# Kernel optimization log

Measured on AMD Instinct MI355X. Metric: run time of the kernel, lower is better.

Reference implementation:

```python
import jax, jax.numpy as jnp
import numpy as np

NUM_HEADS = 32
HEAD_DIM = 128
LORA_RANK = 512
Q_LORA_RANK = 1536
BSZ = 16
SEQ_LEN = 4096


def setup_inputs() -> dict:
    key = jax.random.key(0)
    k1, k2, k3, k4, k5, k6 = jax.random.split(key, 6)
    hd = NUM_HEADS * HEAD_DIM
    return {
        "hidden_states_q": jax.random.normal(k1, (BSZ, Q_LORA_RANK), dtype=jnp.float32),
        "compressed_kv": jax.random.normal(k2, (BSZ, SEQ_LEN, LORA_RANK), dtype=jnp.float32),
        # nn.Linear params: weight [out, in], bias [out]
        "Wq": jax.random.normal(k3, (hd, Q_LORA_RANK), dtype=jnp.float32) / np.sqrt(Q_LORA_RANK),
        "bq": jax.random.normal(k4, (hd,), dtype=jnp.float32) * 0.01,
        "Wkv": jax.random.normal(k5, (hd, LORA_RANK), dtype=jnp.float32) / np.sqrt(LORA_RANK),
        "bkv": jax.random.normal(k6, (hd,), dtype=jnp.float32) * 0.01,
    }


def reference(hidden_states_q, compressed_kv, Wq, bq, Wkv, bkv):
    bsz = hidden_states_q.shape[0]
    seq_len = compressed_kv.shape[1]
    # q: [b, h, d]
    q = (hidden_states_q @ Wq.T + bq).reshape(bsz, NUM_HEADS, HEAD_DIM)
    # kv decompression: [b, s, h, d] (same tensor used for both K and V)
    kv = (compressed_kv @ Wkv.T + bkv).reshape(bsz, seq_len, NUM_HEADS, HEAD_DIM)
    # attention scores per head over seq (note: original has NO 1/sqrt(d) scaling)
    attn = jnp.einsum('bhd,bshd->bhs', q, kv)
    attn = jax.nn.softmax(attn, axis=-1)
    out = jnp.einsum('bhs,bshd->bhd', attn, kv)
    return out.reshape(bsz, NUM_HEADS * HEAD_DIM)
```

## Files before the change

### kernel.cpp

```cpp
#include <hip/hip_runtime.h>

#define B  16
#define S  4096
#define R  512
#define QR 1536
#define H  32
#define D  128
#define HD 4096
#define SC 128
#define CH 32

using f32x4 = __attribute__((ext_vector_type(4))) float;
using s16x8 = __attribute__((ext_vector_type(8))) short;

__device__ __forceinline__ ushort bf_hi(float x) {
  return (ushort)(__float_as_uint(x) >> 16);
}
__device__ __forceinline__ float bf_res(float x) {
  return x - __uint_as_float(__float_as_uint(x) & 0xFFFF0000u);
}
__device__ __forceinline__ ushort f2bf_rne(float x) {
  uint u = __float_as_uint(x);
  return (ushort)((u + 0x7FFFu + ((u >> 16) & 1u)) >> 16);
}

__global__ __launch_bounds__(512) void k_q(const float* __restrict__ hsq,
                                           const float* __restrict__ Wq,
                                           const float* __restrict__ bq,
                                           float* __restrict__ q) {
  __shared__ float hs[B * QR];
  int tid = threadIdx.x;
  for (int idx = tid * 4; idx < B * QR; idx += 2048)
    *(float4*)&hs[idx] = *(const float4*)&hsq[idx];
  __syncthreads();

  int wave = tid >> 6, lane = tid & 63;
  int o = blockIdx.x * 16 + wave * 2;

  float acc0[B], acc1[B];
#pragma unroll
  for (int b = 0; b < B; ++b) { acc0[b] = 0.f; acc1[b] = 0.f; }

  const float* w0r = Wq + (size_t)o * QR;
  const float* w1r = w0r + QR;
  for (int k = lane * 4; k < QR; k += 256) {
    float4 wa = *(const float4*)&w0r[k];
    float4 wb = *(const float4*)&w1r[k];
#pragma unroll
    for (int b = 0; b < B; ++b) {
      float4 h4 = *(const float4*)&hs[b * QR + k];
      acc0[b] += wa.x * h4.x + wa.y * h4.y + wa.z * h4.z + wa.w * h4.w;
      acc1[b] += wb.x * h4.x + wb.y * h4.y + wb.z * h4.z + wb.w * h4.w;
    }
  }
#pragma unroll
  for (int b = 0; b < B; ++b) {
    float v0 = acc0[b], v1 = acc1[b];
#pragma unroll
    for (int off = 32; off > 0; off >>= 1) {
      v0 += __shfl_xor(v0, off);
      v1 += __shfl_xor(v1, off);
    }
    if (lane == 0) {
      q[b * HD + o]     = v0 + bq[o];
      q[b * HD + o + 1] = v1 + bq[o + 1];
    }
  }
}

__global__ __launch_bounds__(256) void k_qhat(const float* __restrict__ q,
                                              const float* __restrict__ Wkv,
                                              float* __restrict__ qhat) {
  int h = blockIdx.x;
  int r0 = blockIdx.y * 64;
  __shared__ float qs[B][D];
  int tid = threadIdx.x;
  for (int idx = tid; idx < B * D; idx += 256) {
    int b = idx >> 7, d = idx & (D - 1);
    qs[b][d] = q[b * HD + h * D + d];
  }
  __syncthreads();

  int r_l = tid & 63, bg = tid >> 6;
  float acc[4] = {0.f, 0.f, 0.f, 0.f};
  const float* wbase = Wkv + (size_t)(h * D) * R + r0 + r_l;
  for (int d = 0; d < D; d += 4) {
    float w0 = wbase[(d + 0) * R];
    float w1 = wbase[(d + 1) * R];
    float w2 = wbase[(d + 2) * R];
    float w3 = wbase[(d + 3) * R];
#pragma unroll
    for (int i = 0; i < 4; ++i) {
      float4 q4 = *(const float4*)&qs[bg * 4 + i][d];
      acc[i] += q4.x * w0 + q4.y * w1 + q4.z * w2 + q4.w * w3;
    }
  }
#pragma unroll
  for (int i = 0; i < 4; ++i)
    qhat[((size_t)(bg * 4 + i) * H + h) * R + r0 + r_l] = acc[i];
}

__global__ __launch_bounds__(256) void k_fmha(const float* __restrict__ qhat,
                                              const float* __restrict__ ckv,
                                              float* __restrict__ part,
                                              float* __restrict__ mbuf,
                                              float* __restrict__ lbuf) {
  __shared__ __align__(16) ushort cs1h[SC * 64];
  __shared__ __align__(16) ushort cs1l[SC * 64];
  __shared__ __align__(16) float  Ls[H * 132];
  __shared__ __align__(16) ushort Ps[H * 128];
  __shared__ __align__(16) ushort cs2[64 * SC];

  const int b = blockIdx.x, chunk = blockIdx.y;
  const int tid = threadIdx.x;
  const int lane = tid & 63, w = tid >> 6;
  const float* cbase = ckv + ((size_t)b * S + (size_t)chunk * SC) * R;
  const float* qbase = qhat + (size_t)b * H * R;

  f32x4 acc[2][2];
#pragma unroll
  for (int i = 0; i < 2; ++i)
#pragma unroll
    for (int j = 0; j < 2; ++j) acc[i][j] = {0.f, 0.f, 0.f, 0.f};

  const int st_s = tid >> 1;
  const int st_kh = (tid & 1) * 32;

  for (int kt = 0; kt < R; kt += 64) {
    {
      const float* src = cbase + (size_t)st_s * R + kt + st_kh;
#pragma unroll
      for (int j = 0; j < 8; ++j) {
        float4 v = *(const float4*)(src + 4 * j);
        int k0 = st_kh + 4 * j;
        int idx = st_s * 64 + (((k0 >> 3) ^ (st_s & 7)) << 3) + (k0 & 7);
        *(uint*)&cs1h[idx]     = (uint)bf_hi(v.x) | ((uint)bf_hi(v.y) << 16);
        *(uint*)&cs1h[idx + 2] = (uint)bf_hi(v.z) | ((uint)bf_hi(v.w) << 16);
        *(uint*)&cs1l[idx]     = (uint)bf_hi(bf_res(v.x)) | ((uint)bf_hi(bf_res(v.y)) << 16);
        *(uint*)&cs1l[idx + 2] = (uint)bf_hi(bf_res(v.z)) | ((uint)bf_hi(bf_res(v.w)) << 16);
      }
    }
    __syncthreads();
#pragma unroll
    for (int ks = 0; ks < 2; ++ks) {
      const int kk = kt + ks * 32 + (lane >> 4) * 8;
      s16x8 ah[2], al[2], bh[2], bl[2];
#pragma unroll
      for (int mt = 0; mt < 2; ++mt) {
        const float* qp = qbase + (size_t)((lane & 15) + 16 * mt) * R + kk;
        float4 q0 = *(const float4*)qp;
        float4 q1 = *(const float4*)(qp + 4);
        float qv[8] = {q0.x, q0.y, q0.z, q0.w, q1.x, q1.y, q1.z, q1.w};
        s16x8 th, tl;
#pragma unroll
        for (int e = 0; e < 8; ++e) {
          th[e] = (short)bf_hi(qv[e]);
          tl[e] = (short)bf_hi(bf_res(qv[e]));
        }
        ah[mt] = th; al[mt] = tl;
      }
#pragma unroll
      for (int ntl = 0; ntl < 2; ++ntl) {
        int sf = (lane & 15) + 32 * w + 16 * ntl;
        int kb = ks * 4 + (lane >> 4);
        int idx = sf * 64 + ((kb ^ (sf & 7)) << 3);
        bh[ntl] = *(s16x8*)&cs1h[idx];
        bl[ntl] = *(s16x8*)&cs1l[idx];
      }
#pragma unroll
      for (int mt = 0; mt < 2; ++mt)
#pragma unroll
        for (int ntl = 0; ntl < 2; ++ntl) {
          acc[mt][ntl] = __builtin_amdgcn_mfma_f32_16x16x32_bf16(ah[mt], bh[ntl], acc[mt][ntl], 0, 0, 0);
          acc[mt][ntl] = __builtin_amdgcn_mfma_f32_16x16x32_bf16(ah[mt], bl[ntl], acc[mt][ntl], 0, 0, 0);
          acc[mt][ntl] = __builtin_amdgcn_mfma_f32_16x16x32_bf16(al[mt], bh[ntl], acc[mt][ntl], 0, 0, 0);
        }
    }
    __syncthreads();
  }

#pragma unroll
  for (int mt = 0; mt < 2; ++mt)
#pragma unroll
    for (int ntl = 0; ntl < 2; ++ntl)
#pragma unroll
      for (int i = 0; i < 4; ++i) {
        int row = 16 * mt + (lane >> 4) * 4 + i;
        int col = 32 * w + 16 * ntl + (lane & 15);
        Ls[row * 132 + col] = acc[mt][ntl][i];
      }
  __syncthreads();

  {
    const int h = tid >> 3, sl = tid & 7;
    float vals[16];
    float m = -3.0e38f;
#pragma unroll
    for (int k = 0; k < 16; ++k) {
      vals[k] = Ls[h * 132 + sl + 8 * k];
      m = fmaxf(m, vals[k]);
    }
    m = fmaxf(m, __shfl_xor(m, 1));
    m = fmaxf(m, __shfl_xor(m, 2));
    m = fmaxf(m, __shfl_xor(m, 4));
    float sum = 0.f;
#pragma unroll
    for (int k = 0; k < 16; ++k) {
      float e = __expf(vals[k] - m);
      sum += e;
      Ps[h * 128 + ((k ^ (h & 7)) << 3) + sl] = f2bf_rne(e);
    }
    sum += __shfl_xor(sum, 1);
    sum += __shfl_xor(sum, 2);
    sum += __shfl_xor(sum, 4);
    if (sl == 0) {
      mbuf[((size_t)b * CH + chunk) * H + h] = m;
      lbuf[((size_t)b * CH + chunk) * H + h] = sum;
    }
  }
  __syncthreads();

  s16x8 bp[4][2];
#pragma unroll
  for (int kt = 0; kt < 4; ++kt)
#pragma unroll
    for (int nt = 0; nt < 2; ++nt) {
      int h = 16 * nt + (lane & 15);
      int kb = kt * 4 + (lane >> 4);
      bp[kt][nt] = *(s16x8*)&Ps[h * 128 + ((kb ^ (h & 7)) << 3)];
    }

  float* pb = part + (size_t)(b * CH + chunk) * H * R;
  const int b7 = tid & 7, sp = tid >> 3;

  for (int rt = 0; rt < 8; ++rt) {
    const int r0 = rt * 64;
#pragma unroll
    for (int so = 0; so < 2; ++so) {
      int s = 2 * sp + 64 * so;
      const float* row0 = cbase + (size_t)s * R + r0;
      const float* row1 = row0 + R;
#pragma unroll
      for (int i = 0; i < 8; ++i) {
        int r = b7 + 8 * i;
        int idx = r * 128 + (((s >> 3) ^ (r & 7)) << 3) + (s & 7);
        *(uint*)&cs2[idx] = (uint)f2bf_rne(row0[r]) | ((uint)f2bf_rne(row1[r]) << 16);
      }
    }
    __syncthreads();

    f32x4 acc2[2];
    acc2[0] = {0.f, 0.f, 0.f, 0.f};
    acc2[1] = {0.f, 0.f, 0.f, 0.f};
    const int rl = 16 * w + (lane & 15);
#pragma unroll
    for (int kt = 0; kt < 4; ++kt) {
      int kb = kt * 4 + (lane >> 4);
      s16x8 a2 = *(s16x8*)&cs2[rl * 128 + ((kb ^ (rl & 7)) << 3)];
#pragma unroll
      for (int nt = 0; nt < 2; ++nt)
        acc2[nt] = __builtin_amdgcn_mfma_f32_16x16x32_bf16(a2, bp[kt][nt], acc2[nt], 0, 0, 0);
    }
#pragma unroll
    for (int nt = 0; nt < 2; ++nt) {
      int h = 16 * nt + (lane & 15);
#pragma unroll
      for (int i = 0; i < 4; ++i) {
        int rg = r0 + 16 * w + (lane >> 4) * 4 + i;
        pb[(size_t)h * R + rg] = acc2[nt][i];
      }
    }
    __syncthreads();
  }
}

__global__ __launch_bounds__(256) void k_combine(const float* __restrict__ part,
                                                 const float* __restrict__ mbuf,
                                                 const float* __restrict__ lbuf,
                                                 float* __restrict__ ctx) {
  const int bid = blockIdx.x;
  const int b = bid >> 5, h = bid & 31;
  const int tid = threadIdx.x;
  float mv[CH], wv[CH];
  float M = -3.0e38f;
#pragma unroll
  for (int c = 0; c < CH; ++c) {
    mv[c] = mbuf[((size_t)b * CH + c) * H + h];
    M = fmaxf(M, mv[c]);
  }
  float denom = 0.f;
#pragma unroll
  for (int c = 0; c < CH; ++c) {
    wv[c] = __expf(mv[c] - M);
    denom += wv[c] * lbuf[((size_t)b * CH + c) * H + h];
  }
  const float inv = 1.f / denom;
  float s0 = 0.f, s1 = 0.f;
#pragma unroll
  for (int c = 0; c < CH; ++c) {
    const float* pp = part + (((size_t)b * CH + c) * H + h) * R;
    s0 += wv[c] * pp[tid];
    s1 += wv[c] * pp[tid + 256];
  }
  ctx[((size_t)b * H + h) * R + tid] = s0 * inv;
  ctx[((size_t)b * H + h) * R + tid + 256] = s1 * inv;
}

__global__ __launch_bounds__(256) void k_out(const float* __restrict__ ctx,
                                             const float* __restrict__ Wkv,
                                             const float* __restrict__ bkv,
                                             float* __restrict__ out) {
  int h = blockIdx.x;
  int d0 = blockIdx.y * 32;
  __shared__ float cs[B][R];
  int tid = threadIdx.x;
  for (int idx = tid * 4; idx < B * R; idx += 1024) {
    int b = idx >> 9, r = idx & 511;
    *(float4*)&cs[b][r] = *(const float4*)&ctx[(size_t)(b * H + h) * R + r];
  }
  __syncthreads();

  int dg = tid & 31;
  int bg = tid >> 5;
  int d = d0 + dg;
  int b0 = bg * 2;
  float acc0 = 0.f, acc1 = 0.f;
  const float* wrow = Wkv + ((size_t)(h * D + d)) * R;
  for (int i = 0; i < R; i += 4) {
    float4 w4 = *(const float4*)&wrow[i];
    float4 ca = *(const float4*)&cs[b0][i];
    float4 cb = *(const float4*)&cs[b0 + 1][i];
    acc0 += w4.x * ca.x + w4.y * ca.y + w4.z * ca.z + w4.w * ca.w;
    acc1 += w4.x * cb.x + w4.y * cb.y + w4.z * cb.z + w4.w * cb.w;
  }
  float bv = bkv[h * D + d];
  out[(size_t)b0 * HD + h * D + d]       = acc0 + bv;
  out[(size_t)(b0 + 1) * HD + h * D + d] = acc1 + bv;
}

extern "C" void kernel_launch(void* const* d_in, const int* in_sizes, int n_in,
                              void* d_out, int out_size, void* d_ws, size_t ws_size,
                              hipStream_t stream) {
  (void)in_sizes; (void)n_in; (void)out_size; (void)ws_size;
  const float* hsq = (const float*)d_in[0];
  const float* ckv = (const float*)d_in[1];
  const float* Wq  = (const float*)d_in[2];
  const float* bq  = (const float*)d_in[3];
  const float* Wkv = (const float*)d_in[4];
  const float* bkv = (const float*)d_in[5];
  float* out = (float*)d_out;

  float* ws   = (float*)d_ws;
  float* q    = ws;
  float* qhat = q + 65536;
  float* ctx  = qhat + 262144;
  float* mbuf = ctx + 262144;
  float* lbuf = mbuf + (size_t)B * CH * H;
  float* part = lbuf + (size_t)B * CH * H;

  k_q<<<256, 512, 0, stream>>>(hsq, Wq, bq, q);
  k_qhat<<<dim3(32, 8), 256, 0, stream>>>(q, Wkv, qhat);
  k_fmha<<<dim3(B, CH), 256, 0, stream>>>(qhat, ckv, part, mbuf, lbuf);
  k_combine<<<B * H, 256, 0, stream>>>(part, mbuf, lbuf, ctx);
  k_out<<<dim3(32, 4), 256, 0, stream>>>(ctx, Wkv, bkv, out);
}
```

Before: 106.3 us.

## Restructure fused attention kernel: 512 threads, register prefetch, bf16 partials

The attention kernel grows to 512 threads per block. The next K-tile and V-tile are prefetched into registers while the current tile is computed, and q is staged once per tile through shared memory in split bf16 instead of being reconverted by every wave. Softmax now uses in-register shuffle reductions instead of a shared-memory score matrix, and LDS buffers are aliased to save space. Partial outputs are stored as bf16 to halve the write and read traffic between the attention and combine kernels, which adds rounding error to the partial sums.

```diff
diff --git a/kernel.cpp b/kernel.cpp
--- a/kernel.cpp
+++ b/kernel.cpp
@@ -22,6 +22,9 @@
 __device__ __forceinline__ ushort f2bf_rne(float x) {
   uint u = __float_as_uint(x);
   return (ushort)((u + 0x7FFFu + ((u >> 16) & 1u)) >> 16);
+}
+__device__ __forceinline__ float bf2f(ushort u) {
+  return __uint_as_float((uint)u << 16);
 }
 
 __global__ __launch_bounds__(512) void k_q(const float* __restrict__ hsq,
@@ -100,181 +103,230 @@
     qhat[((size_t)(bg * 4 + i) * H + h) * R + r0 + r_l] = acc[i];
 }
 
-__global__ __launch_bounds__(256) void k_fmha(const float* __restrict__ qhat,
-                                              const float* __restrict__ ckv,
-                                              float* __restrict__ part,
-                                              float* __restrict__ mbuf,
-                                              float* __restrict__ lbuf) {
-  __shared__ __align__(16) ushort cs1h[SC * 64];
-  __shared__ __align__(16) ushort cs1l[SC * 64];
-  __shared__ __align__(16) float  Ls[H * 132];
+__global__ __launch_bounds__(512, 4) void k_fmha(const float* __restrict__ qhat,
+                                                 const float* __restrict__ ckv,
+                                                 ushort* __restrict__ part,
+                                                 float* __restrict__ mbuf,
+                                                 float* __restrict__ lbuf) {
+  __shared__ __align__(16) ushort smem[24576];
   __shared__ __align__(16) ushort Ps[H * 128];
-  __shared__ __align__(16) ushort cs2[64 * SC];
+
+  ushort* cs1h = smem;
+  ushort* cs1l = smem + 8192;
+  ushort* qsh  = smem + 16384;
+  ushort* qsl  = smem + 20480;
+  float*  redm = (float*)(smem + 8192);
+  float*  redl = redm + 256;
+  ushort* cs2  = smem;
 
   const int b = blockIdx.x, chunk = blockIdx.y;
   const int tid = threadIdx.x;
   const int lane = tid & 63, w = tid >> 6;
+  const int lcol = lane & 15, lgrp = lane >> 4;
   const float* cbase = ckv + ((size_t)b * S + (size_t)chunk * SC) * R;
   const float* qbase = qhat + (size_t)b * H * R;
 
-  f32x4 acc[2][2];
-#pragma unroll
-  for (int i = 0; i < 2; ++i)
-#pragma unroll
-    for (int j = 0; j < 2; ++j) acc[i][j] = {0.f, 0.f, 0.f, 0.f};
-
-  const int st_s = tid >> 1;
-  const int st_kh = (tid & 1) * 32;
+  const int st_s = tid >> 2;
+  const int st_k = (tid & 3) * 16;
+  const int qrow = tid >> 4;
+  const int qk   = (tid & 15) * 4;
+
+  f32x4 acc[2];
+  acc[0] = {0.f, 0.f, 0.f, 0.f};
+  acc[1] = {0.f, 0.f, 0.f, 0.f};
+
+  float4 v[4], vq;
+  {
+    const float* src = cbase + (size_t)st_s * R + st_k;
+#pragma unroll
+    for (int j = 0; j < 4; ++j) v[j] = *(const float4*)(src + 4 * j);
+    vq = *(const float4*)(qbase + (size_t)qrow * R + qk);
+  }
 
   for (int kt = 0; kt < R; kt += 64) {
+#pragma unroll
+    for (int j = 0; j < 4; ++j) {
+      int k0 = st_k + 4 * j;
+      int idx = st_s * 64 + (((k0 >> 3) ^ (st_s & 7)) << 3) + (k0 & 7);
+      float4 t = v[j];
+      *(uint*)&cs1h[idx]     = (uint)bf_hi(t.x) | ((uint)bf_hi(t.y) << 16);
+      *(uint*)&cs1h[idx + 2] = (uint)bf_hi(t.z) | ((uint)bf_hi(t.w) << 16);
+      *(uint*)&cs1l[idx]     = (uint)bf_hi(bf_res(t.x)) | ((uint)bf_hi(bf_res(t.y)) << 16);
+      *(uint*)&cs1l[idx + 2] = (uint)bf_hi(bf_res(t.z)) | ((uint)bf_hi(bf_res(t.w)) << 16);
+    }
     {
-      const float* src = cbase + (size_t)st_s * R + kt + st_kh;
-#pragma unroll
-      for (int j = 0; j < 8; ++j) {
-        float4 v = *(const float4*)(src + 4 * j);
-        int k0 = st_kh + 4 * j;
-        int idx = st_s * 64 + (((k0 >> 3) ^ (st_s & 7)) << 3) + (k0 & 7);
-        *(uint*)&cs1h[idx]     = (uint)bf_hi(v.x) | ((uint)bf_hi(v.y) << 16);
-        *(uint*)&cs1h[idx + 2] = (uint)bf_hi(v.z) | ((uint)bf_hi(v.w) << 16);
-        *(uint*)&cs1l[idx]     = (uint)bf_hi(bf_res(v.x)) | ((uint)bf_hi(bf_res(v.y)) << 16);
-        *(uint*)&cs1l[idx + 2] = (uint)bf_hi(bf_res(v.z)) | ((uint)bf_hi(bf_res(v.w)) << 16);
+      int idx = qrow * 64 + (((qk >> 3) ^ (qrow & 7)) << 3) + (qk & 7);
+      *(uint*)&qsh[idx]     = (uint)bf_hi(vq.x) | ((uint)bf_hi(vq.y) << 16);
+      *(uint*)&qsh[idx + 2] = (uint)bf_hi(vq.z) | ((uint)bf_hi(vq.w) << 16);
+      *(uint*)&qsl[idx]     = (uint)bf_hi(bf_res(vq.x)) | ((uint)bf_hi(bf_res(vq.y)) << 16);
+      *(uint*)&qsl[idx + 2] = (uint)bf_hi(bf_res(vq.z)) | ((uint)bf_hi(bf_res(vq.w)) << 16);
+    }
+    __syncthreads();
+    if (kt + 64 < R) {
+      const float* src = cbase + (size_t)st_s * R + (kt + 64) + st_k;
+#pragma unroll
+      for (int j = 0; j < 4; ++j) v[j] = *(const float4*)(src + 4 * j);
+      vq = *(const float4*)(qbase + (size_t)qrow * R + (kt + 64) + qk);
+    }
+#pragma unroll
+    for (int ks = 0; ks < 2; ++ks) {
+      const int kb = ks * 4 + lgrp;
+      s16x8 ah[2], al[2], bh, bl;
+#pragma unroll
+      for (int mt = 0; mt < 2; ++mt) {
+        int m = 16 * mt + lcol;
+        int idx = m * 64 + ((kb ^ (m & 7)) << 3);
+        ah[mt] = *(s16x8*)&qsh[idx];
+        al[mt] = *(s16x8*)&qsl[idx];
       }
+      {
+        int sf = 16 * w + lcol;
+        int idx = sf * 64 + ((kb ^ (sf & 7)) << 3);
+        bh = *(s16x8*)&cs1h[idx];
+        bl = *(s16x8*)&cs1l[idx];
+      }
+#pragma unroll
+      for (int mt = 0; mt < 2; ++mt) {
+        acc[mt] = __builtin_amdgcn_mfma_f32_16x16x32_bf16(ah[mt], bh, acc[mt], 0, 0, 0);
+        acc[mt] = __builtin_amdgcn_mfma_f32_16x16x32_bf16(ah[mt], bl, acc[mt], 0, 0, 0);
+        acc[mt] = __builtin_amdgcn_mfma_f32_16x16x32_bf16(al[mt], bh, acc[mt], 0, 0, 0);
+      }
     }
     __syncthreads();
-#pragma unroll
-    for (int ks = 0; ks < 2; ++ks) {
-      const int kk = kt + ks * 32 + (lane >> 4) * 8;
-      s16x8 ah[2], al[2], bh[2], bl[2];
-#pragma unroll
-      for (int mt = 0; mt < 2; ++mt) {
-        const float* qp = qbase + (size_t)((lane & 15) + 16 * mt) * R + kk;
-        float4 q0 = *(const float4*)qp;
-        float4 q1 = *(const float4*)(qp + 4);
-        float qv[8] = {q0.x, q0.y, q0.z, q0.w, q1.x, q1.y, q1.z, q1.w};
-        s16x8 th, tl;
-#pragma unroll
-        for (int e = 0; e < 8; ++e) {
-          th[e] = (short)bf_hi(qv[e]);
-          tl[e] = (short)bf_hi(bf_res(qv[e]));
-        }
-        ah[mt] = th; al[mt] = tl;
+  }
+
+  float pm[2][4];
+#pragma unroll
+  for (int mt = 0; mt < 2; ++mt)
+#pragma unroll
+    for (int i = 0; i < 4; ++i) pm[mt][i] = acc[mt][i];
+#pragma unroll
+  for (int off = 1; off <= 8; off <<= 1)
+#pragma unroll
+    for (int mt = 0; mt < 2; ++mt)
+#pragma unroll
+      for (int i = 0; i < 4; ++i)
+        pm[mt][i] = fmaxf(pm[mt][i], __shfl_xor(pm[mt][i], off));
+  if (lcol == 0) {
+#pragma unroll
+    for (int mt = 0; mt < 2; ++mt)
+#pragma unroll
+      for (int i = 0; i < 4; ++i)
+        redm[(16 * mt + lgrp * 4 + i) * 8 + w] = pm[mt][i];
+  }
+  __syncthreads();
+
+  float e_[2][4], ps[2][4];
+#pragma unroll
+  for (int mt = 0; mt < 2; ++mt)
+#pragma unroll
+    for (int i = 0; i < 4; ++i) {
+      int h = 16 * mt + lgrp * 4 + i;
+      float4 r0 = *(float4*)&redm[h * 8];
+      float4 r1 = *(float4*)&redm[h * 8 + 4];
+      float m = fmaxf(fmaxf(fmaxf(r0.x, r0.y), fmaxf(r0.z, r0.w)),
+                      fmaxf(fmaxf(r1.x, r1.y), fmaxf(r1.z, r1.w)));
+      float e = __expf(acc[mt][i] - m);
+      e_[mt][i] = e;
+      ps[mt][i] = e;
+    }
+#pragma unroll
+  for (int off = 1; off <= 8; off <<= 1)
+#pragma unroll
+    for (int mt = 0; mt < 2; ++mt)
+#pragma unroll
+      for (int i = 0; i < 4; ++i)
+        ps[mt][i] += __shfl_xor(ps[mt][i], off);
+  if (lcol == 0) {
+#pragma unroll
+    for (int mt = 0; mt < 2; ++mt)
+#pragma unroll
+      for (int i = 0; i < 4; ++i)
+        redl[(16 * mt + lgrp * 4 + i) * 8 + w] = ps[mt][i];
+  }
+#pragma unroll
+  for (int mt = 0; mt < 2; ++mt)
+#pragma unroll
+    for (int i = 0; i < 4; ++i) {
+      int h = 16 * mt + lgrp * 4 + i;
+      int s = 16 * w + lcol;
+      Ps[h * 128 + (((s >> 3) ^ (h & 7)) << 3) + (s & 7)] = f2bf_rne(e_[mt][i]);
+    }
+  __syncthreads();
+
+  if (w == 0 && lcol == 0) {
+#pragma unroll
+    for (int mt = 0; mt < 2; ++mt)
+#pragma unroll
+      for (int i = 0; i < 4; ++i) {
+        int h = 16 * mt + lgrp * 4 + i;
+        float4 r0 = *(float4*)&redm[h * 8];
+        float4 r1 = *(float4*)&redm[h * 8 + 4];
+        float M = fmaxf(fmaxf(fmaxf(r0.x, r0.y), fmaxf(r0.z, r0.w)),
+                        fmaxf(fmaxf(r1.x, r1.y), fmaxf(r1.z, r1.w)));
+        float4 l0 = *(float4*)&redl[h * 8];
+        float4 l1 = *(float4*)&redl[h * 8 + 4];
+        float L = (l0.x + l0.y + l0.z + l0.w) + (l1.x + l1.y + l1.z + l1.w);
+        mbuf[((size_t)b * CH + chunk) * H + h] = M;
+        lbuf[((size_t)b * CH + chunk) * H + h] = L;
       }
-#pragma unroll
-      for (int ntl = 0; ntl < 2; ++ntl) {
-        int sf = (lane & 15) + 32 * w + 16 * ntl;
-        int kb = ks * 4 + (lane >> 4);
-        int idx = sf * 64 + ((kb ^ (sf & 7)) << 3);
-        bh[ntl] = *(s16x8*)&cs1h[idx];
-        bl[ntl] = *(s16x8*)&cs1l[idx];
+  }
+
+  const int nt = w & 1, mtr = w >> 1;
+  s16x8 bp4[4];
+#pragma unroll
+  for (int kt4 = 0; kt4 < 4; ++kt4) {
+    int h = 16 * nt + lcol;
+    int kb = kt4 * 4 + lgrp;
+    bp4[kt4] = *(s16x8*)&Ps[h * 128 + ((kb ^ (h & 7)) << 3)];
+  }
+
+  const int b7 = tid & 7, sp = tid >> 3;
+  const int s0 = 2 * sp;
+  float ra[8], rb[8];
+  {
+    const float* row0 = cbase + (size_t)s0 * R;
+    const float* row1 = row0 + R;
+#pragma unroll
+    for (int i = 0; i < 8; ++i) { ra[i] = row0[b7 + 8 * i]; rb[i] = row1[b7 + 8 * i]; }
+  }
+  ushort* pb = part + (size_t)(b * CH + chunk) * H * R;
+
+  for (int rt = 0; rt < 8; ++rt) {
+#pragma unroll
+    for (int i = 0; i < 8; ++i) {
+      int r = b7 + 8 * i;
+      int idx = r * 128 + (((s0 >> 3) ^ (r & 7)) << 3) + (s0 & 7);
+      *(uint*)&cs2[idx] = (uint)f2bf_rne(ra[i]) | ((uint)f2bf_rne(rb[i]) << 16);
+    }
+    __syncthreads();
+    if (rt < 7) {
+      const float* row0 = cbase + (size_t)s0 * R + (rt + 1) * 64;
+      const float* row1 = row0 + R;
+#pragma unroll
+      for (int i = 0; i < 8; ++i) { ra[i] = row0[b7 + 8 * i]; rb[i] = row1[b7 + 8 * i]; }
+    }
+    f32x4 acc2 = {0.f, 0.f, 0.f, 0.f};
+    const int rl = 16 * mtr + lcol;
+#pragma unroll
+    for (int kt4 = 0; kt4 < 4; ++kt4) {
+      int kb = kt4 * 4 + lgrp;
+      s16x8 a2 = *(s16x8*)&cs2[rl * 128 + ((kb ^ (rl & 7)) << 3)];
+      acc2 = __builtin_amdgcn_mfma_f32_16x16x32_bf16(a2, bp4[kt4], acc2, 0, 0, 0);
+    }
+    {
+      int h = 16 * nt + lcol;
+#pragma unroll
+      for (int i = 0; i < 4; ++i) {
+        int rg = rt * 64 + 16 * mtr + lgrp * 4 + i;
+        pb[(size_t)h * R + rg] = f2bf_rne(acc2[i]);
       }
-#pragma unroll
-      for (int mt = 0; mt < 2; ++mt)
-#pragma unroll
-        for (int ntl = 0; ntl < 2; ++ntl) {
-          acc[mt][ntl] = __builtin_amdgcn_mfma_f32_16x16x32_bf16(ah[mt], bh[ntl], acc[mt][ntl], 0, 0, 0);
-          acc[mt][ntl] = __builtin_amdgcn_mfma_f32_16x16x32_bf16(ah[mt], bl[ntl], acc[mt][ntl], 0, 0, 0);
-          acc[mt][ntl] = __builtin_amdgcn_mfma_f32_16x16x32_bf16(al[mt], bh[ntl], acc[mt][ntl], 0, 0, 0);
-        }
     }
     __syncthreads();
   }
-
-#pragma unroll
-  for (int mt = 0; mt < 2; ++mt)
-#pragma unroll
-    for (int ntl = 0; ntl < 2; ++ntl)
-#pragma unroll
-      for (int i = 0; i < 4; ++i) {
-        int row = 16 * mt + (lane >> 4) * 4 + i;
-        int col = 32 * w + 16 * ntl + (lane & 15);
-        Ls[row * 132 + col] = acc[mt][ntl][i];
-      }
-  __syncthreads();
-
-  {
-    const int h = tid >> 3, sl = tid & 7;
-    float vals[16];
-    float m = -3.0e38f;
-#pragma unroll
-    for (int k = 0; k < 16; ++k) {
-      vals[k] = Ls[h * 132 + sl + 8 * k];
-      m = fmaxf(m, vals[k]);
-    }
-    m = fmaxf(m, __shfl_xor(m, 1));
-    m = fmaxf(m, __shfl_xor(m, 2));
-    m = fmaxf(m, __shfl_xor(m, 4));
-    float sum = 0.f;
-#pragma unroll
-    for (int k = 0; k < 16; ++k) {
-      float e = __expf(vals[k] - m);
-      sum += e;
-      Ps[h * 128 + ((k ^ (h & 7)) << 3) + sl] = f2bf_rne(e);
-    }
-    sum += __shfl_xor(sum, 1);
-    sum += __shfl_xor(sum, 2);
-    sum += __shfl_xor(sum, 4);
-    if (sl == 0) {
-      mbuf[((size_t)b * CH + chunk) * H + h] = m;
-      lbuf[((size_t)b * CH + chunk) * H + h] = sum;
-    }
-  }
-  __syncthreads();
-
-  s16x8 bp[4][2];
-#pragma unroll
-  for (int kt = 0; kt < 4; ++kt)
-#pragma unroll
-    for (int nt = 0; nt < 2; ++nt) {
-      int h = 16 * nt + (lane & 15);
-      int kb = kt * 4 + (lane >> 4);
-      bp[kt][nt] = *(s16x8*)&Ps[h * 128 + ((kb ^ (h & 7)) << 3)];
-    }
-
-  float* pb = part + (size_t)(b * CH + chunk) * H * R;
-  const int b7 = tid & 7, sp = tid >> 3;
-
-  for (int rt = 0; rt < 8; ++rt) {
-    const int r0 = rt * 64;
-#pragma unroll
-    for (int so = 0; so < 2; ++so) {
-      int s = 2 * sp + 64 * so;
-      const float* row0 = cbase + (size_t)s * R + r0;
-      const float* row1 = row0 + R;
-#pragma unroll
-      for (int i = 0; i < 8; ++i) {
-        int r = b7 + 8 * i;
-        int idx = r * 128 + (((s >> 3) ^ (r & 7)) << 3) + (s & 7);
-        *(uint*)&cs2[idx] = (uint)f2bf_rne(row0[r]) | ((uint)f2bf_rne(row1[r]) << 16);
-      }
-    }
-    __syncthreads();
-
-    f32x4 acc2[2];
-    acc2[0] = {0.f, 0.f, 0.f, 0.f};
-    acc2[1] = {0.f, 0.f, 0.f, 0.f};
-    const int rl = 16 * w + (lane & 15);
-#pragma unroll
-    for (int kt = 0; kt < 4; ++kt) {
-      int kb = kt * 4 + (lane >> 4);
-      s16x8 a2 = *(s16x8*)&cs2[rl * 128 + ((kb ^ (rl & 7)) << 3)];
-#pragma unroll
-      for (int nt = 0; nt < 2; ++nt)
-        acc2[nt] = __builtin_amdgcn_mfma_f32_16x16x32_bf16(a2, bp[kt][nt], acc2[nt], 0, 0, 0);
-    }
-#pragma unroll
-    for (int nt = 0; nt < 2; ++nt) {
-      int h = 16 * nt + (lane & 15);
-#pragma unroll
-      for (int i = 0; i < 4; ++i) {
-        int rg = r0 + 16 * w + (lane >> 4) * 4 + i;
-        pb[(size_t)h * R + rg] = acc2[nt][i];
-      }
-    }
-    __syncthreads();
-  }
-}
-
-__global__ __launch_bounds__(256) void k_combine(const float* __restrict__ part,
+}
+
+__global__ __launch_bounds__(256) void k_combine(const ushort* __restrict__ part,
                                                  const float* __restrict__ mbuf,
                                                  const float* __restrict__ lbuf,
                                                  float* __restrict__ ctx) {
@@ -298,9 +350,9 @@
   float s0 = 0.f, s1 = 0.f;
 #pragma unroll
   for (int c = 0; c < CH; ++c) {
-    const float* pp = part + (((size_t)b * CH + c) * H + h) * R;
-    s0 += wv[c] * pp[tid];
-    s1 += wv[c] * pp[tid + 256];
+    const ushort* pp = part + (((size_t)b * CH + c) * H + h) * R;
+    s0 += wv[c] * bf2f(pp[tid]);
+    s1 += wv[c] * bf2f(pp[tid + 256]);
   }
   ctx[((size_t)b * H + h) * R + tid] = s0 * inv;
   ctx[((size_t)b * H + h) * R + tid + 256] = s1 * inv;
@@ -356,11 +408,11 @@
   float* ctx  = qhat + 262144;
   float* mbuf = ctx + 262144;
   float* lbuf = mbuf + (size_t)B * CH * H;
-  float* part = lbuf + (size_t)B * CH * H;
+  ushort* part = (ushort*)(lbuf + (size_t)B * CH * H);
 
   k_q<<<256, 512, 0, stream>>>(hsq, Wq, bq, q);
   k_qhat<<<dim3(32, 8), 256, 0, stream>>>(q, Wkv, qhat);
-  k_fmha<<<dim3(B, CH), 256, 0, stream>>>(qhat, ckv, part, mbuf, lbuf);
+  k_fmha<<<dim3(B, CH), 512, 0, stream>>>(qhat, ckv, part, mbuf, lbuf);
   k_combine<<<B * H, 256, 0, stream>>>(part, mbuf, lbuf, ctx);
   k_out<<<dim3(32, 4), 256, 0, stream>>>(ctx, Wkv, bkv, out);
 }
```

After: 90.73 us. -14.7%, faster.
